# Kernel tuning notes

Measured on AMD Instinct MI355X. Metric: run time of the kernel, lower is better.

The kernel has to match this reference:

```python
import jax, jax.numpy as jnp
import numpy as np

BINS = 10
LOSS_WEIGHT = 1.0
N, C = 524288, 80


def setup_inputs() -> dict:
    key = jax.random.key(0)
    k1, k2 = jax.random.split(key)
    pred = jax.random.normal(k1, (N, C), dtype=jnp.float32)
    target = jax.random.randint(k2, (N, C), 0, 2).astype(jnp.float32)
    label_weight = jnp.ones((N, C), dtype=jnp.float32)
    return {"pred": pred, "target": target, "label_weight": label_weight}


def reference(pred, target, label_weight):
    # gradient magnitude g = |sigmoid(pred).detach() - target|, in [0, 1)
    g = jnp.abs(jax.nn.sigmoid(jax.lax.stop_gradient(pred)) - target)
    valid = (label_weight > 0)
    validf = valid.astype(pred.dtype)
    tot = jnp.maximum(jnp.sum(validf), 1.0)

    # edges[i] = i/BINS (last edge nudged by 1e-6) -> bin index = floor(g*BINS), clipped
    idx = jnp.clip(jnp.floor(g * BINS).astype(jnp.int32), 0, BINS - 1)
    counts = jnp.zeros((BINS,), dtype=pred.dtype).at[idx.ravel()].add(validf.ravel())
    nonempty = counts > 0
    n = jnp.sum(nonempty.astype(pred.dtype))

    w_per_bin = jnp.where(nonempty, tot / jnp.maximum(counts, 1.0), 0.0)
    weights = w_per_bin[idx] * validf
    weights = weights / jnp.maximum(n, 1.0)
    weights = jax.lax.stop_gradient(weights)  # weights carry no grad in the original

    # binary_cross_entropy_with_logits, elementwise, stable form
    bce = jnp.maximum(pred, 0.0) - pred * target + jnp.log1p(jnp.exp(-jnp.abs(pred)))
    loss = jnp.sum(weights * bce) / tot
    return loss * LOSS_WEIGHT
```

## Files before the change

### kernel.cpp

```cpp
#include <hip/hip_runtime.h>
#include <math.h>

#define BINS 10
#define NBLOCKS 2048
#define THREADS 256

struct Partial {
    float        sum[BINS];
    unsigned int cnt[BINS];
};

__device__ __constant__ const float TH[9] = {
    -2.1972245773f, -1.3862943611f, -0.8472978604f, -0.4054651081f, 0.0f,
     0.4054651081f,  0.8472978604f,  1.3862943611f,  2.1972245773f
};

__device__ __forceinline__ void accum_one(float x, float t, float w,
                                          float (&A)[BINS], unsigned int (&C)[BINS]) {
    float m2t = -2.0f * t;
    float s   = __builtin_fmaf(m2t, x, x);
    float ax  = __builtin_fabsf(x);
    float e   = __expf(-ax);
    float lg  = __logf(1.0f + e);
    float bce = fmaxf(s, 0.0f) + lg;
    bool valid = (w > 0.0f);
    bce = valid ? bce : 0.0f;
    float sv = valid ? s : -1e30f;
    A[0] += bce;
    C[0] += (unsigned int)__popcll(__ballot(valid));
#pragma unroll
    for (int k = 1; k < BINS; ++k) {
        bool m = (sv >= TH[k - 1]);
        A[k] += m ? bce : 0.0f;
        C[k] += (unsigned int)__popcll(__ballot(m));
    }
}

__device__ __forceinline__ void accum4(const float4& p, const float4& t, const float4& w,
                                       float (&A)[BINS], unsigned int (&C)[BINS]) {
    accum_one(p.x, t.x, w.x, A, C);
    accum_one(p.y, t.y, w.y, A, C);
    accum_one(p.z, t.z, w.z, A, C);
    accum_one(p.w, t.w, w.w, A, C);
}

__global__ __launch_bounds__(THREADS) void ghmc_main(const float* __restrict__ pred,
                                                     const float* __restrict__ target,
                                                     const float* __restrict__ lw,
                                                     Partial* __restrict__ part,
                                                     long long total) {
    float        A[BINS];
    unsigned int C[BINS];
#pragma unroll
    for (int b = 0; b < BINS; ++b) { A[b] = 0.0f; C[b] = 0u; }

    const int tid = threadIdx.x;
    const long long nvec   = total >> 2;
    const long long stride = (long long)gridDim.x * THREADS;
    const float4* __restrict__ P = reinterpret_cast<const float4*>(pred);
    const float4* __restrict__ T = reinterpret_cast<const float4*>(target);
    const float4* __restrict__ W = reinterpret_cast<const float4*>(lw);

    long long i = (long long)blockIdx.x * THREADS + tid;
    const bool have = (i < nvec);
    float4 pa, ta, wa;
    if (have) { pa = P[i]; ta = T[i]; wa = W[i]; }
    for (long long j = i + stride; j < nvec; j += stride) {
        float4 pb = P[j], tb = T[j], wb = W[j];
        accum4(pa, ta, wa, A, C);
        pa = pb; ta = tb; wa = wb;
    }
    if (have) accum4(pa, ta, wa, A, C);

    const long long base = nvec << 2;
    const int rem = (int)(total - base);
    if (blockIdx.x == 0 && tid < rem)
        accum_one(pred[base + tid], target[base + tid], lw[base + tid], A, C);

#pragma unroll
    for (int b = 0; b < BINS; ++b) {
#pragma unroll
        for (int off = 32; off; off >>= 1)
            A[b] += __shfl_xor(A[b], off, 64);
    }

    __shared__ float        ls[THREADS / 64][BINS];
    __shared__ unsigned int lc[THREADS / 64][BINS];
    const int wid  = tid >> 6;
    const int lane = tid & 63;
    if (lane == 0) {
#pragma unroll
        for (int b = 0; b < BINS; ++b) { ls[wid][b] = A[b]; lc[wid][b] = C[b]; }
    }
    __syncthreads();

    if (tid < BINS) {
        float sb = 0.0f; unsigned int cb = 0u;
#pragma unroll
        for (int w2 = 0; w2 < THREADS / 64; ++w2) { sb += ls[w2][tid]; cb += lc[w2][tid]; }
        part[blockIdx.x].sum[tid] = sb;
        part[blockIdx.x].cnt[tid] = cb;
    }
}

__global__ __launch_bounds__(THREADS) void ghmc_finalize(const Partial* __restrict__ part,
                                                         float* __restrict__ out,
                                                         int nblocks) {
    double             acc[BINS];
    unsigned long long cn[BINS];
#pragma unroll
    for (int b = 0; b < BINS; ++b) { acc[b] = 0.0; cn[b] = 0ull; }

    const int tid = threadIdx.x;
    for (int i = tid; i < nblocks; i += THREADS) {
#pragma unroll
        for (int b = 0; b < BINS; ++b) {
            acc[b] += (double)part[i].sum[b];
            cn[b]  += (unsigned long long)part[i].cnt[b];
        }
    }
#pragma unroll
    for (int b = 0; b < BINS; ++b) {
#pragma unroll
        for (int off = 32; off; off >>= 1) {
            acc[b] += __shfl_xor(acc[b], off, 64);
            cn[b]  += __shfl_xor(cn[b], off, 64);
        }
    }

    __shared__ double             lds_s[THREADS / 64][BINS];
    __shared__ unsigned long long lds_c[THREADS / 64][BINS];
    const int wid  = tid >> 6;
    const int lane = tid & 63;
    if (lane == 0) {
#pragma unroll
        for (int b = 0; b < BINS; ++b) { lds_s[wid][b] = acc[b]; lds_c[wid][b] = cn[b]; }
    }
    __syncthreads();

    if (tid == 0) {
        double pS[BINS + 1];
        double pC[BINS + 1];
        for (int b = 0; b < BINS; ++b) {
            double sb = 0.0; unsigned long long cb = 0ull;
            for (int w2 = 0; w2 < THREADS / 64; ++w2) { sb += lds_s[w2][b]; cb += lds_c[w2][b]; }
            pS[b] = sb; pC[b] = (double)cb;
        }
        pS[BINS] = 0.0; pC[BINS] = 0.0;
        double loss = 0.0;
        int n = 0;
        for (int b = 0; b < BINS; ++b) {
            double cb = pC[b] - pC[b + 1];
            double sb = pS[b] - pS[b + 1];
            if (cb > 0.0) { loss += sb / cb; ++n; }
        }
        double denom = (n > 0) ? (double)n : 1.0;
        out[0] = (float)(loss / denom);
    }
}

extern "C" void kernel_launch(void* const* d_in, const int* in_sizes, int n_in,
                              void* d_out, int out_size, void* d_ws, size_t ws_size,
                              hipStream_t stream) {
    const float* pred   = (const float*)d_in[0];
    const float* target = (const float*)d_in[1];
    const float* lw     = (const float*)d_in[2];
    float* out = (float*)d_out;
    Partial* part = (Partial*)d_ws;
    const long long total = (long long)in_sizes[0];

    ghmc_main<<<NBLOCKS, THREADS, 0, stream>>>(pred, target, lw, part, total);
    ghmc_finalize<<<1, THREADS, 0, stream>>>(part, out, NBLOCKS);
}
```

Measured before the change: 437.0 us.

## Add all-valid fast path, double-buffer loads two strides ahead, halve grid

Adds a wave-uniform fast path for groups where every label weight is positive. It skips the validity select and the first-bin ballot and adds a constant 64 to the first count instead. The main loop now prefetches two strided float4 groups per iteration instead of one, so more loads are in flight. The grid is halved to 1024 blocks and occupancy is hinted with launch bounds. The cost is higher register pressure and fewer resident waves to hide memory latency.

```diff
diff --git a/kernel.cpp b/kernel.cpp
--- a/kernel.cpp
+++ b/kernel.cpp
@@ -2,7 +2,7 @@
 #include <math.h>
 
 #define BINS 10
-#define NBLOCKS 2048
+#define NBLOCKS 1024
 #define THREADS 256
 
 struct Partial {
@@ -15,14 +15,28 @@
      0.4054651081f,  0.8472978604f,  1.3862943611f,  2.1972245773f
 };
 
-__device__ __forceinline__ void accum_one(float x, float t, float w,
-                                          float (&A)[BINS], unsigned int (&C)[BINS]) {
-    float m2t = -2.0f * t;
-    float s   = __builtin_fmaf(m2t, x, x);
+__device__ __forceinline__ void accum_fast(float x, float t,
+                                           float (&A)[BINS], unsigned int (&C)[BINS]) {
+    float s   = __builtin_fmaf(-2.0f * t, x, x);
     float ax  = __builtin_fabsf(x);
     float e   = __expf(-ax);
-    float lg  = __logf(1.0f + e);
-    float bce = fmaxf(s, 0.0f) + lg;
+    float bce = fmaxf(s, 0.0f) + __logf(1.0f + e);
+    A[0] += bce;
+    C[0] += 64u;
+#pragma unroll
+    for (int k = 1; k < BINS; ++k) {
+        bool m = (s >= TH[k - 1]);
+        A[k] += m ? bce : 0.0f;
+        C[k] += (unsigned int)__popcll(__ballot(m));
+    }
+}
+
+__device__ __forceinline__ void accum_slow(float x, float t, float w,
+                                           float (&A)[BINS], unsigned int (&C)[BINS]) {
+    float s   = __builtin_fmaf(-2.0f * t, x, x);
+    float ax  = __builtin_fabsf(x);
+    float e   = __expf(-ax);
+    float bce = fmaxf(s, 0.0f) + __logf(1.0f + e);
     bool valid = (w > 0.0f);
     bce = valid ? bce : 0.0f;
     float sv = valid ? s : -1e30f;
@@ -38,17 +52,25 @@
 
 __device__ __forceinline__ void accum4(const float4& p, const float4& t, const float4& w,
                                        float (&A)[BINS], unsigned int (&C)[BINS]) {
-    accum_one(p.x, t.x, w.x, A, C);
-    accum_one(p.y, t.y, w.y, A, C);
-    accum_one(p.z, t.z, w.z, A, C);
-    accum_one(p.w, t.w, w.w, A, C);
-}
-
-__global__ __launch_bounds__(THREADS) void ghmc_main(const float* __restrict__ pred,
-                                                     const float* __restrict__ target,
-                                                     const float* __restrict__ lw,
-                                                     Partial* __restrict__ part,
-                                                     long long total) {
+    float mw = fminf(fminf(w.x, w.y), fminf(w.z, w.w));
+    if (__all(mw > 0.0f)) {
+        accum_fast(p.x, t.x, A, C);
+        accum_fast(p.y, t.y, A, C);
+        accum_fast(p.z, t.z, A, C);
+        accum_fast(p.w, t.w, A, C);
+    } else {
+        accum_slow(p.x, t.x, w.x, A, C);
+        accum_slow(p.y, t.y, w.y, A, C);
+        accum_slow(p.z, t.z, w.z, A, C);
+        accum_slow(p.w, t.w, w.w, A, C);
+    }
+}
+
+__global__ __launch_bounds__(THREADS, 4) void ghmc_main(const float* __restrict__ pred,
+                                                        const float* __restrict__ target,
+                                                        const float* __restrict__ lw,
+                                                        Partial* __restrict__ part,
+                                                        long long total) {
     float        A[BINS];
     unsigned int C[BINS];
 #pragma unroll
@@ -56,26 +78,36 @@
 
     const int tid = threadIdx.x;
     const long long nvec   = total >> 2;
-    const long long stride = (long long)gridDim.x * THREADS;
+    const long long stride = (long long)NBLOCKS * THREADS;
     const float4* __restrict__ P = reinterpret_cast<const float4*>(pred);
     const float4* __restrict__ T = reinterpret_cast<const float4*>(target);
     const float4* __restrict__ W = reinterpret_cast<const float4*>(lw);
 
     long long i = (long long)blockIdx.x * THREADS + tid;
-    const bool have = (i < nvec);
-    float4 pa, ta, wa;
-    if (have) { pa = P[i]; ta = T[i]; wa = W[i]; }
-    for (long long j = i + stride; j < nvec; j += stride) {
-        float4 pb = P[j], tb = T[j], wb = W[j];
-        accum4(pa, ta, wa, A, C);
-        pa = pb; ta = tb; wa = wb;
-    }
-    if (have) accum4(pa, ta, wa, A, C);
+    if (i + stride < nvec) {
+        float4 pa0 = P[i], ta0 = T[i], wa0 = W[i];
+        float4 pa1 = P[i + stride], ta1 = T[i + stride], wa1 = W[i + stride];
+        i += 2 * stride;
+        for (; i + stride < nvec; i += 2 * stride) {
+            float4 pb0 = P[i], tb0 = T[i], wb0 = W[i];
+            float4 pb1 = P[i + stride], tb1 = T[i + stride], wb1 = W[i + stride];
+            accum4(pa0, ta0, wa0, A, C);
+            accum4(pa1, ta1, wa1, A, C);
+            pa0 = pb0; ta0 = tb0; wa0 = wb0;
+            pa1 = pb1; ta1 = tb1; wa1 = wb1;
+        }
+        accum4(pa0, ta0, wa0, A, C);
+        accum4(pa1, ta1, wa1, A, C);
+    }
+    for (; i < nvec; i += stride) {
+        float4 p = P[i], t = T[i], w = W[i];
+        accum4(p, t, w, A, C);
+    }
 
     const long long base = nvec << 2;
     const int rem = (int)(total - base);
     if (blockIdx.x == 0 && tid < rem)
-        accum_one(pred[base + tid], target[base + tid], lw[base + tid], A, C);
+        accum_slow(pred[base + tid], target[base + tid], lw[base + tid], A, C);
 
 #pragma unroll
     for (int b = 0; b < BINS; ++b) {
```

New measurement: 441.6 us. About the same (+1.1%).
